# Performance work log

Hardware: AMD Instinct MI355X
Metric: run time of the kernel (lower is better)

Reference implementation:

```python
import jax, jax.numpy as jnp
import numpy as np

S = 2   # upsample scale
K = 5   # reassembly kernel k_up


def setup_inputs() -> dict:
    key = jax.random.key(0)
    ks = jax.random.split(key, 7)
    B, C, H, W = 4, 128, 64, 64
    C_MID = 64
    return {
        "x": jax.random.normal(ks[0], (B, C, H, W), dtype=jnp.float32),
        "w1": jax.random.normal(ks[1], (C_MID, C), dtype=jnp.float32) * 0.05,
        "w2": jax.random.normal(ks[2], (S * S * K * K, C_MID, 3, 3), dtype=jnp.float32) * 0.05,
        "bn_gamma": jax.random.uniform(ks[3], (C_MID,), dtype=jnp.float32, minval=0.5, maxval=1.5),
        "bn_beta": jax.random.normal(ks[4], (C_MID,), dtype=jnp.float32) * 0.1,
        "bn_mean": jax.random.normal(ks[5], (C_MID,), dtype=jnp.float32) * 0.1,
        "bn_var": jax.random.uniform(ks[6], (C_MID,), dtype=jnp.float32, minval=0.5, maxval=1.5),
    }


def reference(x, w1, w2, bn_gamma, bn_beta, bn_mean, bn_var):
    B, C, H, W = x.shape
    s, k = S, K
    eps = 1e-5
    # --- content encoder: 1x1 conv -> BN (inference form) -> ReLU -> 3x3 conv ---
    h = jnp.einsum('bchw,oc->bohw', x, w1)  # (B, c_mid, H, W)
    inv = bn_gamma / jnp.sqrt(bn_var + eps)
    h = h * inv[None, :, None, None] + (bn_beta - bn_mean * inv)[None, :, None, None]
    h = jax.nn.relu(h)
    ker = jax.lax.conv_general_dilated(
        h, w2, window_strides=(1, 1), padding=((1, 1), (1, 1)),
        dimension_numbers=('NCHW', 'OIHW', 'NCHW'))  # (B, s*s*k*k, H, W)
    # softmax over the k*k reassembly window
    ker = jax.nn.softmax(ker.reshape(B, s * s, k * k, H, W), axis=2)
    # --- unfold k x k neighborhoods of x (row-major window order, as F.unfold) ---
    p = k // 2
    xp = jnp.pad(x, ((0, 0), (0, 0), (p, p), (p, p)))
    patches = jnp.stack(
        [xp[:, :, i:i + H, j:j + W] for i in range(k) for j in range(k)],
        axis=2)  # (B, C, k*k, H, W)
    # weighted reassembly: sum over the k*k window per (sub-pixel, channel)
    out = jnp.einsum('bckhw,bskhw->bcshw', patches, ker)  # (B, C, s*s, H, W)
    # pixel shuffle: (B, C, s, s, H, W) -> (B, C, H*s, W*s)
    out = out.reshape(B, C, s, s, H, W).transpose(0, 1, 4, 2, 5, 3)
    return out.reshape(B, C, H * s, W * s)
```

## Files before the change

kernel.cpp:

```cpp
#include <hip/hip_runtime.h>
#include <hip/hip_bf16.h>

#define HW 4096

typedef __attribute__((ext_vector_type(8))) short  short8;
typedef __attribute__((ext_vector_type(4))) float  floatx4;

#define OFF_W2B 0ul
#define OFF_W1B 129024ul
#define OFF_BN  145408ul
#define OFF_XG  145920ul

__device__ __forceinline__ float bfbits(unsigned u) {
    union { unsigned u; float f; } t; t.u = u; return t.f;
}

__global__ __launch_bounds__(256) void prep_kernel(const float* __restrict__ x,
                                                   const float* __restrict__ w1,
                                                   const float* __restrict__ w2,
                                                   const float* __restrict__ gamma,
                                                   const float* __restrict__ beta,
                                                   const float* __restrict__ mean,
                                                   const float* __restrict__ var,
                                                   char* __restrict__ ws) {
    int tid = blockIdx.x * 256 + threadIdx.x;
    if (tid < 262144) {
        int pix = tid & 4095;
        int cq  = (tid >> 12) & 15;
        int b   = tid >> 16;
        const float* xp = x + ((size_t)(b * 128 + cq * 8)) * HW + pix;
        union { short8 s; __hip_bfloat16 h[8]; } u;
        #pragma unroll
        for (int cc = 0; cc < 8; ++cc) u.h[cc] = __float2bfloat16(xp[(size_t)cc * HW]);
        *(short8*)((__hip_bfloat16*)(ws + OFF_XG) + (size_t)tid * 8) = u.s;
        return;
    }
    int t2 = tid - 262144;
    if (t2 < 64512) {
        int n = t2 / 576;
        int k = t2 - n * 576;
        int t = k >> 6, c = k & 63;
        float v = (n < 100) ? w2[(n * 64 + c) * 9 + t] : 0.f;
        ((__hip_bfloat16*)(ws + OFF_W2B))[t2] = __float2bfloat16(v);
    } else if (t2 < 64512 + 8192) {
        int i = t2 - 64512;
        ((__hip_bfloat16*)(ws + OFF_W1B))[i] = __float2bfloat16(w1[i]);
    } else if (t2 < 64512 + 8192 + 64) {
        int o = t2 - 64512 - 8192;
        float inv = gamma[o] * rsqrtf(var[o] + 1e-5f);
        ((float2*)(ws + OFF_BN))[o] = make_float2(inv, beta[o] - mean[o] * inv);
    }
}

__global__ __launch_bounds__(512, 8) void fused_carafe(const char* __restrict__ ws,
                                                       float* __restrict__ out) {
    __shared__ __align__(16) char smem[30480];
    __hip_bfloat16* xs = (__hip_bfloat16*)smem;
    float*          lg = (float*)(smem + 16384);
    __hip_bfloat16* hs = (__hip_bfloat16*)(smem + 23680);
    float*          ks = (float*)(smem + 23680);

    int b    = blockIdx.x >> 8;
    int tile = blockIdx.x & 255;
    int ty0 = (tile >> 4) * 4;
    int tx0 = (tile & 15) * 4;
    int tid = threadIdx.x;
    int lane = tid & 63, wave = tid >> 6;
    int q = lane >> 4, m = lane & 15;

    const __hip_bfloat16* xg = (const __hip_bfloat16*)(ws + OFF_XG) + (size_t)b * 16 * 4096 * 8;
    #pragma unroll
    for (int it = 0; it < 2; ++it) {
        int idx = tid + it * 512;
        int cq = idx >> 6, p = idx & 63;
        int gy = ty0 + (p >> 3) - 2, gx = tx0 + (p & 7) - 2;
        short8 v;
        #pragma unroll
        for (int j = 0; j < 8; ++j) v[j] = 0;
        if ((unsigned)gy < 64u && (unsigned)gx < 64u)
            v = *(const short8*)(xg + ((size_t)cq * 4096 + gy * 64 + gx) * 8);
        *(short8*)(xs + (size_t)idx * 8) = v;
    }
    __syncthreads();

    {
        const __hip_bfloat16* w1b = (const __hip_bfloat16*)(ws + OFF_W1B);
        for (int task = wave; task < 12; task += 8) {
            int mt = task >> 2, nt = task & 3;
            int bo = nt * 16 + m;
            float2 bnia = ((const float2*)(ws + OFF_BN))[bo];
            int hp = mt * 16 + m;
            int hpc = (hp < 36) ? hp : 0;
            int hy1 = hpc / 6, hx1 = hpc - hy1 * 6;
            int xrow = (hy1 + 1) * 8 + (hx1 + 1);
            floatx4 acc;
            #pragma unroll
            for (int r = 0; r < 4; ++r) acc[r] = 0.f;
            #pragma unroll
            for (int s = 0; s < 4; ++s) {
                short8 a  = *(const short8*)(xs + ((size_t)(s * 4 + q) * 64 + xrow) * 8);
                short8 bw = *(const short8*)(w1b + bo * 128 + s * 32 + q * 8);
                acc = __builtin_amdgcn_mfma_f32_16x16x32_bf16(a, bw, acc, 0, 0, 0);
            }
            #pragma unroll
            for (int r = 0; r < 4; ++r) {
                int prow = mt * 16 + q * 4 + r;
                if (prow < 36) {
                    int phy = prow / 6, phx = prow - phy * 6;
                    int gy = ty0 + phy - 1, gx = tx0 + phx - 1;
                    bool in = ((unsigned)gy < 64u) && ((unsigned)gx < 64u);
                    float v = in ? fmaxf(fmaf(acc[r], bnia.x, bnia.y), 0.f) : 0.f;
                    hs[prow * 72 + bo] = __float2bfloat16(v);
                }
            }
        }
    }
    __syncthreads();

    if (wave < 7) {
        int nt = wave;
        int py = m >> 2, px = m & 3;
        const __hip_bfloat16* w2b = (const __hip_bfloat16*)(ws + OFF_W2B);
        const __hip_bfloat16* bp  = w2b + (size_t)(nt * 16 + m) * 576 + q * 8;

        floatx4 acc;
        #pragma unroll
        for (int r = 0; r < 4; ++r) acc[r] = 0.f;

        short8 bcur = *(const short8*)bp;
        for (int s = 0; s < 18; ++s) {
            int t = s >> 1, c0 = (s & 1) * 32;
            int ti = t / 3, tj = t - ti * 3;
            short8 a = *(const short8*)(hs + ((size_t)((py + ti) * 6 + px + tj)) * 72 + c0 + q * 8);
            short8 bn2 = bcur;
            if (s < 17) bn2 = *(const short8*)(bp + (s + 1) * 32);
            acc = __builtin_amdgcn_mfma_f32_16x16x32_bf16(a, bcur, acc, 0, 0, 0);
            bcur = bn2;
        }
        #pragma unroll
        for (int r = 0; r < 4; ++r)
            lg[(q * 4 + r) * 114 + nt * 16 + m] = acc[r];
    }
    __syncthreads();

    if (tid < 64) {
        int pix = tid & 15, g = tid >> 4;
        float v[25];
        #pragma unroll
        for (int wi = 0; wi < 25; ++wi) v[wi] = lg[pix * 114 + g * 25 + wi];
        float mx = v[0];
        #pragma unroll
        for (int wi = 1; wi < 25; ++wi) mx = fmaxf(mx, v[wi]);
        float ssum = 0.f;
        #pragma unroll
        for (int wi = 0; wi < 25; ++wi) { v[wi] = __expf(v[wi] - mx); ssum += v[wi]; }
        float rs = 1.f / ssum;
        #pragma unroll
        for (int t25 = 0; t25 < 25; ++t25)
            ks[(t25 * 4 + g) * 17 + pix] = v[t25] * rs;
    }
    __syncthreads();

    {
        int pix = lane & 15, g4 = lane >> 4;
        int py = pix >> 2, px = pix & 3;
        int Y = ty0 + py, X = tx0 + px;
        int gy = g4 >> 1, gx = g4 & 1;
        float* op = out + ((((size_t)b * 128) * 128 + (2 * Y + gy)) * 128 + 2 * X + gx);

        for (int co = wave; co < 16; co += 8) {
            float acc[8];
            #pragma unroll
            for (int i = 0; i < 8; ++i) acc[i] = 0.f;

            const __hip_bfloat16* xsb = xs + (size_t)co * 64 * 8;
            #pragma unroll 5
            for (int t = 0; t < 25; ++t) {
                int ti = t / 5, tj = t - ti * 5;
                int xrow = (py + ti) * 8 + (px + tj);
                union { short8 s; unsigned u[4]; } xv;
                xv.s = *(const short8*)(xsb + xrow * 8);
                float k = ks[(t * 4 + g4) * 17 + pix];
                #pragma unroll
                for (int j = 0; j < 4; ++j) {
                    float xa  = bfbits(xv.u[j] << 16);
                    float xb2 = bfbits(xv.u[j] & 0xFFFF0000u);
                    acc[j * 2 + 0] = fmaf(xa,  k, acc[j * 2 + 0]);
                    acc[j * 2 + 1] = fmaf(xb2, k, acc[j * 2 + 1]);
                }
            }

            #pragma unroll
            for (int i = 0; i < 8; ++i)
                op[(size_t)(co * 8 + i) << 14] = acc[i];
        }
    }
}

extern "C" void kernel_launch(void* const* d_in, const int* in_sizes, int n_in,
                              void* d_out, int out_size, void* d_ws, size_t ws_size,
                              hipStream_t stream) {
    const float* x     = (const float*)d_in[0];
    const float* w1    = (const float*)d_in[1];
    const float* w2    = (const float*)d_in[2];
    const float* gamma = (const float*)d_in[3];
    const float* beta  = (const float*)d_in[4];
    const float* mean  = (const float*)d_in[5];
    const float* var   = (const float*)d_in[6];
    float* out = (float*)d_out;
    char*  ws  = (char*)d_ws;

    prep_kernel<<<1309, 256, 0, stream>>>(x, w1, w2, gamma, beta, mean, var, ws);
    fused_carafe<<<1024, 512, 0, stream>>>(ws, out);
}
```

Before: 117.0 us.

## Compute CARAFE reassembly with MFMA via split-bf16 kernel weights and padded x layout

The scalar FMA reassembly loop becomes bf16 MFMA matmuls. Softmax weights are scattered into a banded 64x64 matrix, split into hi and lo bf16 parts to keep precision, and multiplied against a channel-major x tile. The prep kernel now also writes a zero-padded bf16 copy of x. The 1x1 conv reads its input directly from global memory instead of shared memory. XOR swizzling is applied to the shared-memory layouts to avoid bank conflicts. In exchange the prep kernel writes more global data, the MFMAs do extra multiplies on the zero entries of the banded matrix, and a shared-memory zeroing pass plus barrier is added.

```diff
diff --git a/kernel.cpp b/kernel.cpp
--- a/kernel.cpp
+++ b/kernel.cpp
@@ -5,15 +5,13 @@
 
 typedef __attribute__((ext_vector_type(8))) short  short8;
 typedef __attribute__((ext_vector_type(4))) float  floatx4;
+typedef __attribute__((ext_vector_type(4))) unsigned short ushort4v;
 
 #define OFF_W2B 0ul
 #define OFF_W1B 129024ul
 #define OFF_BN  145408ul
 #define OFF_XG  145920ul
-
-__device__ __forceinline__ float bfbits(unsigned u) {
-    union { unsigned u; float f; } t; t.u = u; return t.f;
-}
+#define OFF_XPP 4340224ul
 
 __global__ __launch_bounds__(256) void prep_kernel(const float* __restrict__ x,
                                                    const float* __restrict__ w1,
@@ -49,16 +47,35 @@
         int o = t2 - 64512 - 8192;
         float inv = gamma[o] * rsqrtf(var[o] + 1e-5f);
         ((float2*)(ws + OFF_BN))[o] = make_float2(inv, beta[o] - mean[o] * inv);
+    } else {
+        int t3 = t2 - 72768;
+        if (t3 < 591872) {
+            int j  = t3 % 17;
+            int rr = t3 / 17;
+            int row68 = rr - (rr / 68) * 68;
+            int bc = rr / 68;
+            int gy = row68 - 2;
+            const float* xp = x + (size_t)bc * HW + (size_t)gy * 64;
+            union { ushort4v u4; __hip_bfloat16 h[4]; } u;
+            #pragma unroll
+            for (int e = 0; e < 4; ++e) {
+                int gx = j * 4 + e - 2;
+                float f = 0.f;
+                if ((unsigned)gy < 64u && (unsigned)gx < 64u) f = xp[gx];
+                u.h[e] = __float2bfloat16(f);
+            }
+            *(ushort4v*)((__hip_bfloat16*)(ws + OFF_XPP) + (size_t)rr * 68 + j * 4) = u.u4;
+        }
     }
 }
 
 __global__ __launch_bounds__(512, 8) void fused_carafe(const char* __restrict__ ws,
                                                        float* __restrict__ out) {
-    __shared__ __align__(16) char smem[30480];
-    __hip_bfloat16* xs = (__hip_bfloat16*)smem;
-    float*          lg = (float*)(smem + 16384);
-    __hip_bfloat16* hs = (__hip_bfloat16*)(smem + 23680);
-    float*          ks = (float*)(smem + 23680);
+    __shared__ __align__(16) char smem[40064];
+    __hip_bfloat16* xsT = (__hip_bfloat16*)smem;
+    float*          lg  = (float*)(smem + 16384);
+    __hip_bfloat16* hs  = (__hip_bfloat16*)(smem + 23680);
+    __hip_bfloat16* Whi = (__hip_bfloat16*)(smem + 23680);
 
     int b    = blockIdx.x >> 8;
     int tile = blockIdx.x & 255;
@@ -68,22 +85,20 @@
     int lane = tid & 63, wave = tid >> 6;
     int q = lane >> 4, m = lane & 15;
 
-    const __hip_bfloat16* xg = (const __hip_bfloat16*)(ws + OFF_XG) + (size_t)b * 16 * 4096 * 8;
+    const __hip_bfloat16* xpp = (const __hip_bfloat16*)(ws + OFF_XPP);
     #pragma unroll
     for (int it = 0; it < 2; ++it) {
         int idx = tid + it * 512;
-        int cq = idx >> 6, p = idx & 63;
-        int gy = ty0 + (p >> 3) - 2, gx = tx0 + (p & 7) - 2;
-        short8 v;
-        #pragma unroll
-        for (int j = 0; j < 8; ++j) v[j] = 0;
-        if ((unsigned)gy < 64u && (unsigned)gx < 64u)
-            v = *(const short8*)(xg + ((size_t)cq * 4096 + gy * 64 + gx) * 8);
-        *(short8*)(xs + (size_t)idx * 8) = v;
-    }
-    __syncthreads();
+        int c = idx >> 3, h = idx & 7;
+        size_t rb = ((size_t)(b * 128 + c) * 68 + (ty0 + h)) * 68 + tx0;
+        union { short8 s; uint2 d[2]; } u;
+        u.d[0] = *(const uint2*)(xpp + rb);
+        u.d[1] = *(const uint2*)(xpp + rb + 4);
+        *(short8*)(xsT + c * 64 + ((h ^ (c & 7)) << 3)) = u.s;
+    }
 
     {
+        const __hip_bfloat16* xg  = (const __hip_bfloat16*)(ws + OFF_XG) + (size_t)b * 16 * 4096 * 8;
         const __hip_bfloat16* w1b = (const __hip_bfloat16*)(ws + OFF_W1B);
         for (int task = wave; task < 12; task += 8) {
             int mt = task >> 2, nt = task & 3;
@@ -92,13 +107,15 @@
             int hp = mt * 16 + m;
             int hpc = (hp < 36) ? hp : 0;
             int hy1 = hpc / 6, hx1 = hpc - hy1 * 6;
-            int xrow = (hy1 + 1) * 8 + (hx1 + 1);
+            int gy = ty0 + hy1 - 1, gx = tx0 + hx1 - 1;
+            int gyc = min(max(gy, 0), 63), gxc = min(max(gx, 0), 63);
+            int pix = gyc * 64 + gxc;
             floatx4 acc;
             #pragma unroll
             for (int r = 0; r < 4; ++r) acc[r] = 0.f;
             #pragma unroll
             for (int s = 0; s < 4; ++s) {
-                short8 a  = *(const short8*)(xs + ((size_t)(s * 4 + q) * 64 + xrow) * 8);
+                short8 a  = *(const short8*)(xg + ((size_t)((s * 4 + q) * 4096 + pix)) * 8);
                 short8 bw = *(const short8*)(w1b + bo * 128 + s * 32 + q * 8);
                 acc = __builtin_amdgcn_mfma_f32_16x16x32_bf16(a, bw, acc, 0, 0, 0);
             }
@@ -107,10 +124,10 @@
                 int prow = mt * 16 + q * 4 + r;
                 if (prow < 36) {
                     int phy = prow / 6, phx = prow - phy * 6;
-                    int gy = ty0 + phy - 1, gx = tx0 + phx - 1;
-                    bool in = ((unsigned)gy < 64u) && ((unsigned)gx < 64u);
+                    int gy2 = ty0 + phy - 1, gx2 = tx0 + phx - 1;
+                    bool in = ((unsigned)gy2 < 64u) && ((unsigned)gx2 < 64u);
                     float v = in ? fmaxf(fmaf(acc[r], bnia.x, bnia.y), 0.f) : 0.f;
-                    hs[prow * 72 + bo] = __float2bfloat16(v);
+                    hs[prow * 64 + ((((bo >> 3) ^ (prow & 7)) << 3) | (bo & 7))] = __float2bfloat16(v);
                 }
             }
         }
@@ -129,9 +146,10 @@
 
         short8 bcur = *(const short8*)bp;
         for (int s = 0; s < 18; ++s) {
-            int t = s >> 1, c0 = (s & 1) * 32;
+            int t = s >> 1, co = (s & 1) * 4 + q;
             int ti = t / 3, tj = t - ti * 3;
-            short8 a = *(const short8*)(hs + ((size_t)((py + ti) * 6 + px + tj)) * 72 + c0 + q * 8);
+            int row = (py + ti) * 6 + (px + tj);
+            short8 a = *(const short8*)(hs + row * 64 + ((co ^ (row & 7)) << 3));
             short8 bn2 = bcur;
             if (s < 17) bn2 = *(const short8*)(bp + (s + 1) * 32);
             acc = __builtin_amdgcn_mfma_f32_16x16x32_bf16(a, bcur, acc, 0, 0, 0);
@@ -143,11 +161,21 @@
     }
     __syncthreads();
 
+    {
+        short8 z;
+        #pragma unroll
+        for (int j = 0; j < 8; ++j) z[j] = 0;
+        *(short8*)((char*)Whi + tid * 16) = z;
+        *(short8*)((char*)Whi + 8192 + tid * 16) = z;
+    }
+    __syncthreads();
+
     if (tid < 64) {
-        int pix = tid & 15, g = tid >> 4;
+        int pixid = tid >> 2, g = tid & 3;
+        int py = pixid >> 2, px = pixid & 3;
         float v[25];
         #pragma unroll
-        for (int wi = 0; wi < 25; ++wi) v[wi] = lg[pix * 114 + g * 25 + wi];
+        for (int wi = 0; wi < 25; ++wi) v[wi] = lg[pixid * 114 + g * 25 + wi];
         float mx = v[0];
         #pragma unroll
         for (int wi = 1; wi < 25; ++wi) mx = fmaxf(mx, v[wi]);
@@ -155,44 +183,46 @@
         #pragma unroll
         for (int wi = 0; wi < 25; ++wi) { v[wi] = __expf(v[wi] - mx); ssum += v[wi]; }
         float rs = 1.f / ssum;
-        #pragma unroll
-        for (int t25 = 0; t25 < 25; ++t25)
-            ks[(t25 * 4 + g) * 17 + pix] = v[t25] * rs;
+        int row = tid;
+        #pragma unroll
+        for (int t25 = 0; t25 < 25; ++t25) {
+            int ti = t25 / 5, tj = t25 - ti * 5;
+            int addr = row * 64 + ((((py + ti) ^ (row & 7)) << 3) | (px + tj));
+            float kv = v[t25] * rs;
+            __hip_bfloat16 khi = __float2bfloat16(kv);
+            Whi[addr] = khi;
+            Whi[4096 + addr] = __float2bfloat16(kv - __bfloat162float(khi));
+        }
     }
     __syncthreads();
 
     {
-        int pix = lane & 15, g4 = lane >> 4;
-        int py = pix >> 2, px = pix & 3;
-        int Y = ty0 + py, X = tx0 + px;
-        int gy = g4 >> 1, gx = g4 & 1;
-        float* op = out + ((((size_t)b * 128) * 128 + (2 * Y + gy)) * 128 + 2 * X + gx);
-
-        for (int co = wave; co < 16; co += 8) {
-            float acc[8];
-            #pragma unroll
-            for (int i = 0; i < 8; ++i) acc[i] = 0.f;
-
-            const __hip_bfloat16* xsb = xs + (size_t)co * 64 * 8;
-            #pragma unroll 5
-            for (int t = 0; t < 25; ++t) {
-                int ti = t / 5, tj = t - ti * 5;
-                int xrow = (py + ti) * 8 + (px + tj);
-                union { short8 s; unsigned u[4]; } xv;
-                xv.s = *(const short8*)(xsb + xrow * 8);
-                float k = ks[(t * 4 + g4) * 17 + pix];
-                #pragma unroll
-                for (int j = 0; j < 4; ++j) {
-                    float xa  = bfbits(xv.u[j] << 16);
-                    float xb2 = bfbits(xv.u[j] & 0xFFFF0000u);
-                    acc[j * 2 + 0] = fmaf(xa,  k, acc[j * 2 + 0]);
-                    acc[j * 2 + 1] = fmaf(xb2, k, acc[j * 2 + 1]);
-                }
-            }
-
-            #pragma unroll
-            for (int i = 0; i < 8; ++i)
-                op[(size_t)(co * 8 + i) << 14] = acc[i];
+        int nt = wave;
+        int c = nt * 16 + m;
+        const __hip_bfloat16* xr = xsT + c * 64;
+        short8 b0 = *(const short8*)(xr + ((q ^ (c & 7)) << 3));
+        short8 b1 = *(const short8*)(xr + (((4 + q) ^ (c & 7)) << 3));
+        float* outc = out + (((size_t)b * 128 + c) << 14);
+        #pragma unroll
+        for (int mt = 0; mt < 4; ++mt) {
+            int row = mt * 16 + m;
+            const __hip_bfloat16* wr = Whi + row * 64;
+            int s0 = ((q ^ (row & 7)) << 3);
+            int s1 = (((4 + q) ^ (row & 7)) << 3);
+            short8 ah0 = *(const short8*)(wr + s0);
+            short8 al0 = *(const short8*)(wr + 4096 + s0);
+            short8 ah1 = *(const short8*)(wr + s1);
+            short8 al1 = *(const short8*)(wr + 4096 + s1);
+            floatx4 acc;
+            #pragma unroll
+            for (int r = 0; r < 4; ++r) acc[r] = 0.f;
+            acc = __builtin_amdgcn_mfma_f32_16x16x32_bf16(ah0, b0, acc, 0, 0, 0);
+            acc = __builtin_amdgcn_mfma_f32_16x16x32_bf16(al0, b0, acc, 0, 0, 0);
+            acc = __builtin_amdgcn_mfma_f32_16x16x32_bf16(ah1, b1, acc, 0, 0, 0);
+            acc = __builtin_amdgcn_mfma_f32_16x16x32_bf16(al1, b1, acc, 0, 0, 0);
+            float* op = outc + (size_t)(2 * (ty0 + mt)) * 128 + 2 * (tx0 + q);
+            *(float2*)op         = make_float2(acc[0], acc[1]);
+            *(float2*)(op + 128) = make_float2(acc[2], acc[3]);
         }
     }
 }
@@ -210,6 +240,6 @@
     float* out = (float*)d_out;
     char*  ws  = (char*)d_ws;
 
-    prep_kernel<<<1309, 256, 0, stream>>>(x, w1, w2, gamma, beta, mean, var, ws);
+    prep_kernel<<<3621, 256, 0, stream>>>(x, w1, w2, gamma, beta, mean, var, ws);
     fused_carafe<<<1024, 512, 0, stream>>>(ws, out);
 }
```

New measurement: 118.4 us. Within noise of the previous version (+1.2%).
